# Optimization experiments

Hardware: AMD Instinct MI355X
Metric: run time of the kernel (lower is better)

Reference implementation:

```python
import jax, jax.numpy as jnp
from jax import lax
import numpy as np

T, N, C, S = 256, 64, 7356, 32
NEG = -1e9  # finite stand-in for -inf (keeps grads clean)


def setup_inputs() -> dict:
    key = jax.random.key(0)
    k1, k2, k3 = jax.random.split(key, 3)
    out = jax.random.normal(k1, (T, N, C), dtype=jnp.float32)
    # PyTorch CTCLoss expects log-probs; the module passes `out` through as-is,
    # so we feed log_softmax'd activations (what the surrounding model produces).
    out = jax.nn.log_softmax(out, axis=-1)
    text = jax.random.randint(k2, (N, S), 1, C)            # labels in [1, C-1], blank=0 excluded
    pre_len = jnp.full((N,), T, dtype=jnp.int64 if jax.config.jax_enable_x64 else jnp.int32)
    lengths = jax.random.randint(k3, (N,), 16, S + 1)       # target lengths in [16, 32]
    return {"out": out, "text": text, "pre_len": pre_len, "lengths": lengths}


def _ctc_loss_mean(logp, targets, input_lengths, target_lengths):
    # logp: [T, N, C] log-probs; targets: [N, S]; lengths: [N]
    Tt, Nn, _ = logp.shape
    Ss = targets.shape[1]
    L = 2 * Ss + 1
    # Extended label sequence: blank, l1, blank, l2, ..., blank
    ext = jnp.zeros((Nn, L), dtype=targets.dtype).at[:, 1::2].set(targets)  # [N, L]
    ext_m2 = jnp.concatenate([jnp.zeros((Nn, 2), dtype=ext.dtype), ext[:, :-2]], axis=1)
    skip = (jnp.arange(L)[None, :] >= 2) & (ext != 0) & (ext != ext_m2)      # [N, L]

    # Gather per-frame log-probs of extended labels: [T, N, L]
    lp_ext = logp[:, jnp.arange(Nn)[:, None], ext]

    alpha0 = jnp.full((Nn, L), NEG, dtype=logp.dtype)
    alpha0 = alpha0.at[:, 0].set(lp_ext[0, :, 0]).at[:, 1].set(lp_ext[0, :, 1])

    negcol1 = jnp.full((Nn, 1), NEG, dtype=logp.dtype)
    negcol2 = jnp.full((Nn, 2), NEG, dtype=logp.dtype)

    def step(alpha, lp_t):
        s1 = jnp.concatenate([negcol1, alpha[:, :-1]], axis=1)
        s2 = jnp.concatenate([negcol2, alpha[:, :-2]], axis=1)
        a = jnp.logaddexp(alpha, s1)
        a = jnp.logaddexp(a, jnp.where(skip, s2, NEG))
        new = a + lp_t
        return new, new

    _, alphas_rest = lax.scan(step, alpha0, lp_ext[1:])
    alphas = jnp.concatenate([alpha0[None], alphas_rest], axis=0)  # [T, N, L]

    n_idx = jnp.arange(Nn)
    a_end = alphas[input_lengths - 1, n_idx]                        # [N, L]
    l_last = 2 * target_lengths                                     # index of final blank
    log_like = jnp.logaddexp(a_end[n_idx, l_last], a_end[n_idx, l_last - 1])
    # reduction='mean': per-sample loss / target_length, then mean over batch
    per = -log_like / target_lengths.astype(logp.dtype)
    return jnp.mean(per)


def reference(out, text, pre_len, lengths):
    loss = _ctc_loss_mean(out, text, pre_len, lengths)
    weight = jnp.square(1.0 - jnp.exp(-loss))
    return weight * loss
```

## Files before the change

kernel.cpp:

```cpp
#include <hip/hip_runtime.h>

#define Tt 256
#define Nn 64
#define Cc 7356
#define Ss 32
#define NEGf (-1.0e9f)
#define LOG2E 1.4426950408889634f
#define LN2   0.6931471805599453f
#define PFD 16
#define HT 128

__device__ __forceinline__ float fexp2(float x) { return __builtin_amdgcn_exp2f(x); }
__device__ __forceinline__ float flog2(float x) { return __builtin_amdgcn_logf(x); }

__device__ __forceinline__ float dpp_shr1(float x, float fallback) {
    int r = __builtin_amdgcn_update_dpp(__float_as_int(fallback), __float_as_int(x),
                                        0x138 , 0xf, 0xf, false);
    return __int_as_float(r);
}
__device__ __forceinline__ float dpp_shl1(float x, float fallback) {
    int r = __builtin_amdgcn_update_dpp(__float_as_int(fallback), __float_as_int(x),
                                        0x130 , 0xf, 0xf, false);
    return __int_as_float(r);
}
__device__ __forceinline__ float bcast(float x, int l) {
    return __int_as_float(__builtin_amdgcn_readlane(__float_as_int(x), l));
}
__device__ __forceinline__ float lse2(float a, float b) {
    float m = fmaxf(a, b);
    return m + flog2(fexp2(a - m) + fexp2(b - m));
}

#define COMPACT_FLOATS (Tt * Nn * 64)
#define JV_OFF COMPACT_FLOATS
#define WS_NEED_BYTES ((COMPACT_FLOATS + Nn * 132) * 4)

__global__ __launch_bounds__(256) void ctc_gather_kernel(
    const float* __restrict__ logp, const int* __restrict__ text,
    float* __restrict__ compact)
{
    int tid = blockIdx.x * 256 + threadIdx.x;
    int l = tid & 63;
    int n = (tid >> 6) & (Nn - 1);
    int t = tid >> 12;
    int ch = (l & 1) ? 0 : text[n * Ss + (l >> 1)];
    compact[tid] = logp[(size_t)t * (Nn * Cc) + (size_t)n * Cc + ch] * LOG2E;
}

__global__ __launch_bounds__(64) void ctc_fb_kernel(
    const float* __restrict__ compact, const int* __restrict__ text,
    const int* __restrict__ lengths, float* __restrict__ ws)
{
    const int lane = threadIdx.x;
    const int n    = blockIdx.x & (Nn - 1);
    const bool fwd = blockIdx.x < Nn;

    int ch = (lane & 1) ? 0 : text[n * Ss + (lane >> 1)];
    int ch_m2 = __shfl_up(ch, 2, 64);
    int ch_p2 = __shfl_down(ch, 2, 64);
    const bool skipd = (lane >= 2) && !(lane & 1) && (ch != ch_m2);
    const bool skips = !(lane & 1) && (lane <= 61) && (ch != ch_p2);

    const float* base = compact + (size_t)n * 64 + lane;
    const int rstride = Nn * 64;

    float* outv = ws + JV_OFF + n * 132 + (fwd ? 0 : 66);

    float stv;
    float st0;

    if (fwd) {
        float lp0 = base[0];
        stv = (lane == 0) ? lp0 : NEGf;
        st0 = bcast(lp0, 1);
        float lpb[PFD];
        #pragma unroll
        for (int i = 0; i < PFD; ++i)
            lpb[i] = base[(size_t)(1 + i) * rstride];
        int t = 1;
        for (int blk = 0; blk < 7; ++blk) {
            #pragma unroll
            for (int j = 0; j < PFD; ++j) {
                float lp = lpb[j];
                int tpf = t + PFD;
                if (tpf <= HT - 1)
                    lpb[j] = base[(size_t)tpf * rstride];
                float lpblank = bcast(lp, 1);
                float s1 = dpp_shr1(stv, st0);
                float s2 = dpp_shr1(s1, NEGf);
                float s2m = skipd ? s2 : NEGf;
                float m  = fmaxf(fmaxf(stv, s1), s2m);
                float e  = fexp2(stv - m) + fexp2(s1 - m) + fexp2(s2m - m);
                stv = (m + lp) + flog2(e);
                st0 = st0 + lpblank;
                ++t;
            }
        }
        #pragma unroll
        for (int j = 0; j < PFD - 1; ++j) {
            float lp = lpb[j];
            float lpblank = bcast(lp, 1);
            float s1 = dpp_shr1(stv, st0);
            float s2 = dpp_shr1(s1, NEGf);
            float s2m = skipd ? s2 : NEGf;
            float m  = fmaxf(fmaxf(stv, s1), s2m);
            float e  = fexp2(stv - m) + fexp2(s1 - m) + fexp2(s2m - m);
            stv = (m + lp) + flog2(e);
            st0 = st0 + lpblank;
        }
        float s1 = dpp_shr1(stv, st0);
        float s2 = dpp_shr1(s1, NEGf);
        float s2m = skipd ? s2 : NEGf;
        float m  = fmaxf(fmaxf(stv, s1), s2m);
        float e  = fexp2(stv - m) + fexp2(s1 - m) + fexp2(s2m - m);
        outv[1 + lane] = m + flog2(e);
        if (lane == 0) outv[0] = st0;
    } else {
        const int len = lengths[n];
        float lpT = base[(size_t)(Tt - 1) * rstride];
        int llast = 2 * len;
        stv = (lane == llast - 2 || lane == llast - 1) ? lpT : NEGf;
        st0 = NEGf;
        float lpb[PFD];
        #pragma unroll
        for (int i = 0; i < PFD; ++i)
            lpb[i] = base[(size_t)(Tt - 2 - i) * rstride];
        int t = Tt - 2;
        for (int blk = 0; blk < 7; ++blk) {
            #pragma unroll
            for (int j = 0; j < PFD; ++j) {
                float lp = lpb[j];
                int tpf = t - PFD;
                if (tpf >= HT)
                    lpb[j] = base[(size_t)tpf * rstride];
                float lpblank = bcast(lp, 1);
                float b1 = bcast(stv, 0);
                float u1 = dpp_shl1(stv, NEGf);
                float u2 = dpp_shl1(u1, NEGf);
                float u2m = skips ? u2 : NEGf;
                float m  = fmaxf(fmaxf(stv, u1), u2m);
                float e  = fexp2(stv - m) + fexp2(u1 - m) + fexp2(u2m - m);
                float nb = (m + lp) + flog2(e);
                float m2 = fmaxf(st0, b1);
                st0 = (m2 + lpblank) + flog2(fexp2(st0 - m2) + fexp2(b1 - m2));
                stv = nb;
                --t;
            }
        }
        #pragma unroll
        for (int j = 0; j < PFD - 1; ++j) {
            float lp = lpb[j];
            float lpblank = bcast(lp, 1);
            float b1 = bcast(stv, 0);
            float u1 = dpp_shl1(stv, NEGf);
            float u2 = dpp_shl1(u1, NEGf);
            float u2m = skips ? u2 : NEGf;
            float m  = fmaxf(fmaxf(stv, u1), u2m);
            float e  = fexp2(stv - m) + fexp2(u1 - m) + fexp2(u2m - m);
            float nb = (m + lp) + flog2(e);
            float m2 = fmaxf(st0, b1);
            st0 = (m2 + lpblank) + flog2(fexp2(st0 - m2) + fexp2(b1 - m2));
            stv = nb;
        }
        outv[1 + lane] = stv;
        if (lane == 0) outv[0] = st0;
    }
}

__global__ __launch_bounds__(64) void ctc_join_kernel(
    const float* __restrict__ ws, const int* __restrict__ lengths,
    float* __restrict__ out)
{
    const int lane = threadIdx.x;
    const float* va = ws + JV_OFF + lane * 132;
    const float* vb = va + 66;
    float acc = NEGf;
    #pragma unroll 5
    for (int s = 0; s <= 64; ++s)
        acc = lse2(acc, va[s] + vb[s]);
    float per = -(acc * LN2) / (float)lengths[lane];
    #pragma unroll
    for (int off = 32; off > 0; off >>= 1)
        per += __shfl_down(per, off, 64);
    if (lane == 0) {
        float loss = per * (1.0f / (float)Nn);
        float w = 1.0f - __expf(-loss);
        out[0] = w * w * loss;
    }
}

__global__ __launch_bounds__(64) void ctc_alpha_kernel(
    const float* __restrict__ logp, const int* __restrict__ text,
    const int* __restrict__ pre_len, const int* __restrict__ lengths,
    float* __restrict__ per_out)
{
    const int n = blockIdx.x; const int lane = threadIdx.x;
    int ch = 0;
    if (lane & 1) ch = text[n * Ss + (lane >> 1)];
    int ch_m2 = __shfl_up(ch, 2, 64);
    bool skip = (lane >= 2) && (ch != 0) && (ch != ch_m2);
    const size_t rowbase = (size_t)n * Cc, tstride = (size_t)Nn * Cc;
    float lp0 = logp[rowbase + ch] * LOG2E;
    float alpha = (lane < 2) ? lp0 : NEGf, alpha64 = NEGf;
    const int stop_t = pre_len[n] - 1;
    float sv = alpha, sv64 = alpha64;
    float lpb[PFD];
    #pragma unroll
    for (int i = 0; i < PFD; ++i)
        lpb[i] = logp[(size_t)(1 + i) * tstride + rowbase + ch] * LOG2E;
#define CTC_STEP(LPREG) { \
        float lp = (LPREG); float lpblank = bcast(lp, 0); float a63 = bcast(alpha, 63); \
        float s1 = dpp_shr1(alpha, NEGf); float s2 = dpp_shr1(s1, NEGf); \
        float s2m = skip ? s2 : NEGf; \
        float m = fmaxf(fmaxf(alpha, s1), s2m); \
        float e = fexp2(alpha - m) + fexp2(s1 - m) + fexp2(s2m - m); \
        float na = (m + lp) + flog2(e); \
        float m2 = fmaxf(alpha64, a63); \
        alpha64 = (m2 + lpblank) + flog2(fexp2(alpha64 - m2) + fexp2(a63 - m2)); \
        alpha = na; if (t == stop_t) { sv = alpha; sv64 = alpha64; } ++t; }
    int t = 1;
    for (int blk = 0; blk < 15; ++blk) {
        #pragma unroll
        for (int j = 0; j < PFD; ++j) {
            float lpj = lpb[j]; int tpf = t + PFD;
            if (tpf < Tt) lpb[j] = logp[(size_t)tpf * tstride + rowbase + ch] * LOG2E;
            CTC_STEP(lpj);
        }
    }
    #pragma unroll
    for (int j = 0; j < PFD - 1; ++j) { CTC_STEP(lpb[j]); }
#undef CTC_STEP
    int len = lengths[n]; int l_last = 2 * len;
    float v1 = __shfl(sv, l_last < 64 ? l_last : 63, 64);
    if (l_last == 64) v1 = sv64;
    float v2 = __shfl(sv, l_last - 1, 64);
    float per = -(lse2(v1, v2) * LN2) / (float)len;
    if (lane == 0) per_out[n] = per;
}

__global__ __launch_bounds__(64) void finalize_kernel(
    const float* __restrict__ per, float* __restrict__ out)
{
    int lane = threadIdx.x;
    float v = per[lane];
    #pragma unroll
    for (int off = 32; off > 0; off >>= 1) v += __shfl_down(v, off, 64);
    if (lane == 0) {
        float loss = v * (1.0f / (float)Nn);
        float w = 1.0f - __expf(-loss);
        out[0] = w * w * loss;
    }
}

extern "C" void kernel_launch(void* const* d_in, const int* in_sizes, int n_in,
                              void* d_out, int out_size, void* d_ws, size_t ws_size,
                              hipStream_t stream) {
    const float* logp    = (const float*)d_in[0];
    const int*   text    = (const int*)d_in[1];
    const int*   pre_len = (const int*)d_in[2];
    const int*   lengths = (const int*)d_in[3];

    if (ws_size >= (size_t)WS_NEED_BYTES) {
        float* compact = (float*)d_ws;
        ctc_gather_kernel<<<COMPACT_FLOATS / 256, 256, 0, stream>>>(logp, text, compact);
        ctc_fb_kernel<<<2 * Nn, 64, 0, stream>>>(compact, text, lengths, (float*)d_ws);
        ctc_join_kernel<<<1, 64, 0, stream>>>((const float*)d_ws, lengths, (float*)d_out);
    } else {
        float* per = (float*)d_ws;
        ctc_alpha_kernel<<<Nn, 64, 0, stream>>>(logp, text, pre_len, lengths, per);
        finalize_kernel<<<1, 64, 0, stream>>>(per, (float*)d_out);
    }
}
```

Before: 33.34 us.

## Fuse forward/backward and join into one kernel with last-block reduction

```diff
diff --git a/kernel.cpp b/kernel.cpp
--- a/kernel.cpp
+++ b/kernel.cpp
@@ -33,27 +33,45 @@
 
 #define COMPACT_FLOATS (Tt * Nn * 64)
 #define JV_OFF COMPACT_FLOATS
-#define WS_NEED_BYTES ((COMPACT_FLOATS + Nn * 132) * 4)
+#define WS_NEED_BYTES ((COMPACT_FLOATS + Nn + 1) * 4)
 
 __global__ __launch_bounds__(256) void ctc_gather_kernel(
     const float* __restrict__ logp, const int* __restrict__ text,
-    float* __restrict__ compact)
-{
-    int tid = blockIdx.x * 256 + threadIdx.x;
-    int l = tid & 63;
-    int n = (tid >> 6) & (Nn - 1);
-    int t = tid >> 12;
+    float* __restrict__ ws)
+{
+    int gid = blockIdx.x * 256 + threadIdx.x;
+    int l  = gid & 63;
+    int n  = (gid >> 6) & (Nn - 1);
+    int tq = gid >> 12;
     int ch = (l & 1) ? 0 : text[n * Ss + (l >> 1)];
-    compact[tid] = logp[(size_t)t * (Nn * Cc) + (size_t)n * Cc + ch] * LOG2E;
-}
-
-__global__ __launch_bounds__(64) void ctc_fb_kernel(
+    const float* src = logp + (size_t)n * Cc + ch;
+    const size_t tstr = (size_t)Nn * Cc;
+    float v0 = src[(size_t)(4 * tq + 0) * tstr];
+    float v1 = src[(size_t)(4 * tq + 1) * tstr];
+    float v2 = src[(size_t)(4 * tq + 2) * tstr];
+    float v3 = src[(size_t)(4 * tq + 3) * tstr];
+    float* dst = ws + (size_t)n * 64 + l;
+    dst[(size_t)(4 * tq + 0) * (Nn * 64)] = v0 * LOG2E;
+    dst[(size_t)(4 * tq + 1) * (Nn * 64)] = v1 * LOG2E;
+    dst[(size_t)(4 * tq + 2) * (Nn * 64)] = v2 * LOG2E;
+    dst[(size_t)(4 * tq + 3) * (Nn * 64)] = v3 * LOG2E;
+    if (gid == 0) {
+        int* counter = (int*)(ws + JV_OFF + Nn);
+        __hip_atomic_store(counter, 0, __ATOMIC_RELAXED, __HIP_MEMORY_SCOPE_AGENT);
+    }
+}
+
+__global__ __launch_bounds__(128) void ctc_fbj_kernel(
     const float* __restrict__ compact, const int* __restrict__ text,
-    const int* __restrict__ lengths, float* __restrict__ ws)
-{
-    const int lane = threadIdx.x;
-    const int n    = blockIdx.x & (Nn - 1);
-    const bool fwd = blockIdx.x < Nn;
+    const int* __restrict__ lengths, float* __restrict__ ws,
+    float* __restrict__ out)
+{
+    __shared__ float jpre[65];
+    __shared__ float jbeta[65];
+
+    const int lane = threadIdx.x & 63;
+    const bool fwd = threadIdx.x < 64;
+    const int n    = blockIdx.x;
 
     int ch = (lane & 1) ? 0 : text[n * Ss + (lane >> 1)];
     int ch_m2 = __shfl_up(ch, 2, 64);
@@ -63,8 +81,7 @@
 
     const float* base = compact + (size_t)n * 64 + lane;
     const int rstride = Nn * 64;
-
-    float* outv = ws + JV_OFF + n * 132 + (fwd ? 0 : 66);
+    const int len = lengths[n];
 
     float stv;
     float st0;
@@ -113,10 +130,9 @@
         float s2m = skipd ? s2 : NEGf;
         float m  = fmaxf(fmaxf(stv, s1), s2m);
         float e  = fexp2(stv - m) + fexp2(s1 - m) + fexp2(s2m - m);
-        outv[1 + lane] = m + flog2(e);
-        if (lane == 0) outv[0] = st0;
+        jpre[1 + lane] = m + flog2(e);
+        if (lane == 0) jpre[0] = st0;
     } else {
-        const int len = lengths[n];
         float lpT = base[(size_t)(Tt - 1) * rstride];
         int llast = 2 * len;
         stv = (lane == llast - 2 || lane == llast - 1) ? lpT : NEGf;
@@ -162,30 +178,40 @@
             st0 = (m2 + lpblank) + flog2(fexp2(st0 - m2) + fexp2(b1 - m2));
             stv = nb;
         }
-        outv[1 + lane] = stv;
-        if (lane == 0) outv[0] = st0;
-    }
-}
-
-__global__ __launch_bounds__(64) void ctc_join_kernel(
-    const float* __restrict__ ws, const int* __restrict__ lengths,
-    float* __restrict__ out)
-{
-    const int lane = threadIdx.x;
-    const float* va = ws + JV_OFF + lane * 132;
-    const float* vb = va + 66;
-    float acc = NEGf;
-    #pragma unroll 5
-    for (int s = 0; s <= 64; ++s)
-        acc = lse2(acc, va[s] + vb[s]);
-    float per = -(acc * LN2) / (float)lengths[lane];
-    #pragma unroll
-    for (int off = 32; off > 0; off >>= 1)
-        per += __shfl_down(per, off, 64);
+        jbeta[1 + lane] = stv;
+        if (lane == 0) jbeta[0] = st0;
+    }
+
+    __syncthreads();
+    if (!fwd) return;
+
+    float local = jpre[lane] + jbeta[lane];
+    if (lane == 0) local = lse2(local, jpre[64] + jbeta[64]);
+    #pragma unroll
+    for (int off = 1; off < 64; off <<= 1)
+        local = lse2(local, __shfl_xor(local, off, 64));
+    float per = -(local * LN2) / (float)len;
+
+    float* slots = ws + JV_OFF;
+    int* counter = (int*)(ws + JV_OFF + Nn);
+    int old = -1;
     if (lane == 0) {
-        float loss = per * (1.0f / (float)Nn);
-        float w = 1.0f - __expf(-loss);
-        out[0] = w * w * loss;
+        __hip_atomic_store(&slots[n], per, __ATOMIC_RELEASE, __HIP_MEMORY_SCOPE_AGENT);
+        __threadfence();
+        old = __hip_atomic_fetch_add(counter, 1, __ATOMIC_ACQ_REL, __HIP_MEMORY_SCOPE_AGENT);
+    }
+    old = __shfl(old, 0, 64);
+    if (old == Nn - 1) {
+        __threadfence();
+        float v = __hip_atomic_load(&slots[lane], __ATOMIC_ACQUIRE, __HIP_MEMORY_SCOPE_AGENT);
+        #pragma unroll
+        for (int off = 32; off > 0; off >>= 1)
+            v += __shfl_down(v, off, 64);
+        if (lane == 0) {
+            float loss = v * (1.0f / (float)Nn);
+            float w = 1.0f - __expf(-loss);
+            out[0] = w * w * loss;
+        }
     }
 }
 
@@ -261,10 +287,9 @@
     const int*   lengths = (const int*)d_in[3];
 
     if (ws_size >= (size_t)WS_NEED_BYTES) {
-        float* compact = (float*)d_ws;
-        ctc_gather_kernel<<<COMPACT_FLOATS / 256, 256, 0, stream>>>(logp, text, compact);
-        ctc_fb_kernel<<<2 * Nn, 64, 0, stream>>>(compact, text, lengths, (float*)d_ws);
-        ctc_join_kernel<<<1, 64, 0, stream>>>((const float*)d_ws, lengths, (float*)d_out);
+        float* ws = (float*)d_ws;
+        ctc_gather_kernel<<<(Tt / 4) * Nn * 64 / 256, 256, 0, stream>>>(logp, text, ws);
+        ctc_fbj_kernel<<<Nn, 128, 0, stream>>>(ws, text, lengths, ws, (float*)d_out);
     } else {
         float* per = (float*)d_ws;
         ctc_alpha_kernel<<<Nn, 64, 0, stream>>>(logp, text, pre_len, lengths, per);
```

Result: faster. 30.84 us (-7.5%).
